# Kernel tuning notes

Hardware: AMD Instinct MI355X
Metric: run time of the kernel (lower is better)

Reference implementation:

```python
import jax, jax.numpy as jnp
import numpy as np

N = 50000        # nodes
E = 800000       # directed edges (before self-loops)
F_IN = 128       # input node features
HID = 32         # hidden channels per head
HEADS = 4
NCLS = 8
EPS_BN = 1e-5
NEG_SLOPE = 0.2  # GATConv LeakyReLU default


def setup_inputs() -> dict:
    key = jax.random.key(0)
    ks = jax.random.split(key, 16)
    rn = lambda k, shape, s=0.1: jax.random.normal(k, shape, jnp.float32) * s
    inp = {}
    inp["x"] = jax.random.normal(ks[0], (N, F_IN), jnp.float32)
    inp["edge_index"] = jax.random.randint(ks[1], (2, E), 0, N, dtype=jnp.int32)
    # layer 0: F_IN -> HEADS*HID (concat)
    inp["W0"] = rn(ks[2], (F_IN, HEADS * HID))
    inp["as0"] = rn(ks[3], (HEADS, HID))
    inp["ad0"] = rn(ks[4], (HEADS, HID))
    inp["b0"] = jnp.zeros((HEADS * HID,), jnp.float32)
    inp["g0"] = jnp.ones((HEADS * HID,), jnp.float32)
    inp["bb0"] = jnp.zeros((HEADS * HID,), jnp.float32)
    inp["rm0"] = jnp.zeros((HEADS * HID,), jnp.float32)
    inp["rv0"] = jnp.ones((HEADS * HID,), jnp.float32)
    # layer 1: HEADS*HID -> HEADS*HID (concat)
    inp["W1"] = rn(ks[5], (HEADS * HID, HEADS * HID))
    inp["as1"] = rn(ks[6], (HEADS, HID))
    inp["ad1"] = rn(ks[7], (HEADS, HID))
    inp["b1"] = jnp.zeros((HEADS * HID,), jnp.float32)
    inp["g1"] = jnp.ones((HEADS * HID,), jnp.float32)
    inp["bb1"] = jnp.zeros((HEADS * HID,), jnp.float32)
    inp["rm1"] = jnp.zeros((HEADS * HID,), jnp.float32)
    inp["rv1"] = jnp.ones((HEADS * HID,), jnp.float32)
    # layer 2: HEADS*HID -> NCLS, heads=1, concat=False
    inp["W2"] = rn(ks[8], (HEADS * HID, NCLS))
    inp["as2"] = rn(ks[9], (1, NCLS))
    inp["ad2"] = rn(ks[10], (1, NCLS))
    inp["b2"] = jnp.zeros((NCLS,), jnp.float32)
    return inp


def gat_conv(x, src, dst, W, att_s, att_d, bias, H, C, concat):
    """PyG-style GATConv (eval mode, self-loops already appended to src/dst)."""
    n = x.shape[0]
    h = (x @ W).reshape(n, H, C)                       # [N,H,C]
    a_s = (h * att_s).sum(-1)                          # [N,H]
    a_d = (h * att_d).sum(-1)                          # [N,H]
    e = jax.nn.leaky_relu(a_s[src] + a_d[dst], NEG_SLOPE)  # [E,H]
    # numerically-stable segment softmax over incoming edges of each dst node
    m = jax.ops.segment_max(e, dst, num_segments=n)
    m = jnp.where(jnp.isfinite(m), m, 0.0)
    ex = jnp.exp(e - m[dst])
    den = jax.ops.segment_sum(ex, dst, num_segments=n)
    alpha = ex / (den[dst] + 1e-16)                    # [E,H]
    out = jax.ops.segment_sum(h[src] * alpha[:, :, None], dst, num_segments=n)  # [N,H,C]
    out = out.reshape(n, H * C) if concat else out.mean(axis=1)
    return out + bias


def bn_eval(x, g, b, rm, rv):
    return (x - rm) * jax.lax.rsqrt(rv + EPS_BN) * g + b


def reference(x, edge_index, W0, as0, ad0, b0, g0, bb0, rm0, rv0,
              W1, as1, ad1, b1, g1, bb1, rm1, rv1, W2, as2, ad2, b2):
    n = x.shape[0]
    loop = jnp.arange(n, dtype=edge_index.dtype)       # self-loops (PyG default)
    src = jnp.concatenate([edge_index[0], loop])
    dst = jnp.concatenate([edge_index[1], loop])
    h = gat_conv(x, src, dst, W0, as0, ad0, b0, HEADS, HID, True)
    h = jax.nn.elu(bn_eval(h, g0, bb0, rm0, rv0))
    h = gat_conv(h, src, dst, W1, as1, ad1, b1, HEADS, HID, True)
    h = jax.nn.elu(bn_eval(h, g1, bb1, rm1, rv1))
    h = gat_conv(h, src, dst, W2, as2, ad2, b2, 1, NCLS, False)
    return jax.nn.log_softmax(h, axis=1)
```

## Files before the change

kernel.cpp:

```cpp
#include <hip/hip_runtime.h>
#include <math.h>

#define N_NODES 50000
#define N_EDGES 800000
#define ET (N_EDGES + N_NODES)
#define FDIM 128
#define HEADS 4
#define HID 32
#define NCLS 8
#define NEG 0.2f
#define EPS_BN 1e-5f

#define BSH 8
#define NBUCK ((N_NODES + 255) >> BSH)
#define EPB 4096

typedef __attribute__((ext_vector_type(8))) short short8;
typedef __attribute__((ext_vector_type(4))) float f32x4;

__device__ __forceinline__ float lrelu(float e) { return e > 0.f ? e : NEG * e; }
__device__ __forceinline__ float bflo(unsigned u) { return __uint_as_float(u << 16); }
__device__ __forceinline__ float bfhi(unsigned u) { return __uint_as_float(u & 0xffff0000u); }
__device__ __forceinline__ unsigned f2bf(float f) {
    unsigned b = __float_as_uint(f);
    return (b + 0x7fffu + ((b >> 16) & 1u)) >> 16;
}


__global__ void count_deg(const int* __restrict__ ei, int* __restrict__ cnt) {
    int e = blockIdx.x * blockDim.x + threadIdx.x;
    if (e >= ET) return;
    int d = (e < N_EDGES) ? ei[N_EDGES + e] : (e - N_EDGES);
    atomicAdd(&cnt[d], 1);
}

__global__ void scan_partial(const int* __restrict__ cnt, int* __restrict__ offs,
                             int* __restrict__ bsums) {
    __shared__ int s[256];
    int tid = threadIdx.x;
    int i = blockIdx.x * 256 + tid;
    int v = (i < N_NODES) ? cnt[i] : 0;
    s[tid] = v;
    __syncthreads();
    for (int off = 1; off < 256; off <<= 1) {
        int x = (tid >= off) ? s[tid - off] : 0;
        __syncthreads();
        s[tid] += x;
        __syncthreads();
    }
    if (i < N_NODES) offs[i] = s[tid] - v;
    if (tid == 255) bsums[blockIdx.x] = s[255];
}

__global__ void scan_root(const int* __restrict__ bsums, int* __restrict__ boffs, int nb) {
    __shared__ int s[256];
    int tid = threadIdx.x;
    int v = (tid < nb) ? bsums[tid] : 0;
    s[tid] = v;
    __syncthreads();
    for (int off = 1; off < 256; off <<= 1) {
        int x = (tid >= off) ? s[tid - off] : 0;
        __syncthreads();
        s[tid] += x;
        __syncthreads();
    }
    boffs[tid] = s[tid] - v;
}

__global__ void scan_add(int* __restrict__ offs, const int* __restrict__ boffs,
                         const int* __restrict__ bsums, int* __restrict__ bcur, int nb) {
    int i = blockIdx.x * 256 + threadIdx.x;
    if (i < N_NODES) {
        int v = offs[i] + boffs[blockIdx.x];
        offs[i] = v;
        if ((i & ((1 << BSH) - 1)) == 0) bcur[i >> BSH] = v;
    }
    if (i == 0) offs[N_NODES] = boffs[nb - 1] + bsums[nb - 1];
}

__global__ __launch_bounds__(256) void partition_pairs(const int* __restrict__ ei,
                                                       int* __restrict__ bcur,
                                                       int2* __restrict__ pairs) {
    __shared__ unsigned hist[NBUCK];
    __shared__ unsigned base[NBUCK];
    int tid = threadIdx.x;
    int e0 = blockIdx.x * EPB;
    for (int i = tid; i < NBUCK; i += 256) hist[i] = 0;
    __syncthreads();
    #pragma unroll
    for (int k = 0; k < EPB / 256; k++) {
        int e = e0 + k * 256 + tid;
        if (e < ET) {
            int d = (e < N_EDGES) ? ei[N_EDGES + e] : (e - N_EDGES);
            atomicAdd(&hist[d >> BSH], 1u);
        }
    }
    __syncthreads();
    for (int i = tid; i < NBUCK; i += 256) {
        unsigned h = hist[i];
        base[i] = h ? (unsigned)atomicAdd(&bcur[i], (int)h) : 0u;
        hist[i] = 0;
    }
    __syncthreads();
    #pragma unroll
    for (int k = 0; k < EPB / 256; k++) {
        int e = e0 + k * 256 + tid;
        if (e < ET) {
            int s, d;
            if (e < N_EDGES) { s = ei[e]; d = ei[N_EDGES + e]; }
            else             { s = d = e - N_EDGES; }
            int b = d >> BSH;
            unsigned lpos = atomicAdd(&hist[b], 1u);
            pairs[base[b] + lpos] = make_int2(s, d);
        }
    }
}

__global__ __launch_bounds__(256) void group_bucket(const int2* __restrict__ pairs,
                                                    const int* __restrict__ offs,
                                                    int* __restrict__ ssrc) {
    __shared__ int lcur[1 << BSH];
    int b = blockIdx.x, tid = threadIdx.x;
    int n0 = b << BSH;
    int base = offs[n0];
    int nend = n0 + (1 << BSH); if (nend > N_NODES) nend = N_NODES;
    int regionEnd = offs[nend];
    lcur[tid] = (n0 + tid < N_NODES) ? (offs[n0 + tid] - base) : 0;
    __syncthreads();
    for (int i = base + tid; i < regionEnd; i += 256) {
        int2 p = pairs[i];
        int pos = atomicAdd(&lcur[p.y & ((1 << BSH) - 1)], 1);
        ssrc[base + pos] = p.x;
    }
}


#define CAST_B 3125
#define PACK_B 64

__global__ void prep_inputs(const float* __restrict__ x, unsigned short* __restrict__ xb,
                            const float* __restrict__ W0, unsigned short* __restrict__ W0p,
                            const float* __restrict__ W1, unsigned short* __restrict__ W1p) {
    int b = blockIdx.x, tid = threadIdx.x;
    if (b < CAST_B) {
        int i = b * 256 + tid;
        const float4* p = (const float4*)x + (size_t)i * 2;
        float4 a = p[0], c = p[1];
        uint4 o;
        o.x = f2bf(a.x) | (f2bf(a.y) << 16);
        o.y = f2bf(a.z) | (f2bf(a.w) << 16);
        o.z = f2bf(c.x) | (f2bf(c.y) << 16);
        o.w = f2bf(c.z) | (f2bf(c.w) << 16);
        ((uint4*)xb)[i] = o;
    } else {
        int pb = b - CAST_B;
        const float* W = (pb < PACK_B) ? W0 : W1;
        unsigned short* Wp = (pb < PACK_B) ? W0p : W1p;
        int o = (pb & (PACK_B - 1)) * 256 + tid;
        int j = o & 7, lane = (o >> 3) & 63, kc = (o >> 9) & 3, t = o >> 11;
        int k = kc * 32 + ((lane >> 4) << 3) + j;
        int n = t * 16 + (lane & 15);
        Wp[o] = (unsigned short)f2bf(W[k * 128 + n]);
    }
}


__global__ __launch_bounds__(256) void gemm_attn(
        const unsigned short* __restrict__ Ab, const unsigned short* __restrict__ Wp,
        const float* __restrict__ att_s, const float* __restrict__ att_d,
        unsigned short* __restrict__ Hb, float* __restrict__ asn, float* __restrict__ adn,
        int M) {
    __shared__ float tiles[64 * 132];
    int tid = threadIdx.x;
    int wv = tid >> 6, lane = tid & 63;
    int base = blockIdx.x * 64;
    int mrow = base + wv * 16 + (lane & 15);
    if (mrow >= M) mrow = M - 1;
    int koff = (lane >> 4) * 8;

    f32x4 acc[8];
    #pragma unroll
    for (int t = 0; t < 8; t++) acc[t] = (f32x4){0.f, 0.f, 0.f, 0.f};

    #pragma unroll
    for (int kc = 0; kc < 4; kc++) {
        short8 a = *(const short8*)(Ab + (size_t)mrow * 128 + kc * 32 + koff);
        #pragma unroll
        for (int t = 0; t < 8; t++) {
            short8 b = *(const short8*)(Wp + (((t * 4 + kc) * 64 + lane) << 3));
            acc[t] = __builtin_amdgcn_mfma_f32_16x16x32_bf16(a, b, acc[t], 0, 0, 0);
        }
    }

    int rbase = wv * 16 + (lane >> 4) * 4;
    int col = lane & 15;
    #pragma unroll
    for (int t = 0; t < 8; t++)
        #pragma unroll
        for (int r = 0; r < 4; r++)
            tiles[(rbase + r) * 132 + t * 16 + col] = acc[t][r];
    __syncthreads();

    #pragma unroll
    for (int it = 0; it < 4; it++) {
        int u = tid + it * 256;
        int rl = u >> 4, cg = u & 15;
        int row = base + rl;
        if (row < M) {
            const float* p = tiles + rl * 132 + cg * 8;
            float4 v0 = *(const float4*)(p);
            float4 v1 = *(const float4*)(p + 4);
            uint4 o;
            o.x = f2bf(v0.x) | (f2bf(v0.y) << 16);
            o.y = f2bf(v0.z) | (f2bf(v0.w) << 16);
            o.z = f2bf(v1.x) | (f2bf(v1.y) << 16);
            o.w = f2bf(v1.z) | (f2bf(v1.w) << 16);
            *(uint4*)(Hb + (size_t)row * 128 + cg * 8) = o;
        }
    }

    {
        int rl = tid >> 2, hd = tid & 3;
        int row = base + rl;
        if (row < M) {
            const float* hrow = tiles + rl * 132 + hd * 32;
            const float* as = att_s + hd * 32;
            const float* ad = att_d + hd * 32;
            float ps = 0.f, pd = 0.f;
            #pragma unroll
            for (int i = 0; i < 8; i++) {
                float4 hv = *(const float4*)(hrow + i * 4);
                float4 sv = *(const float4*)(as + i * 4);
                float4 dv = *(const float4*)(ad + i * 4);
                ps += hv.x * sv.x + hv.y * sv.y + hv.z * sv.z + hv.w * sv.w;
                pd += hv.x * dv.x + hv.y * dv.y + hv.z * dv.z + hv.w * dv.w;
            }
            asn[row * 4 + hd] = ps;
            adn[row * 4 + hd] = pd;
        }
    }
}


__global__ __launch_bounds__(256) void aggregate(
        const unsigned short* __restrict__ hb, const float* __restrict__ asn,
        const float* __restrict__ adn, const int* __restrict__ offs,
        const int* __restrict__ ssrc, const float* __restrict__ bias,
        const float* __restrict__ gamma, const float* __restrict__ beta,
        const float* __restrict__ rmean, const float* __restrict__ rvar,
        unsigned short* __restrict__ outb) {
    __shared__ int2 sPair[4][4][72];
    int wv = threadIdx.x >> 6;
    int node = blockIdx.x * 4 + wv;
    if (node >= N_NODES) return;
    int lane = threadIdx.x & 63;
    int hd = lane >> 4;
    int beg = offs[node], deg = offs[node + 1] - beg;
    float4 ad4 = *(const float4*)(adn + node * 4);

    if (lane < 32) sPair[wv][lane >> 3][64 + (lane & 7)] = make_int2(0, 0);

    int s0 = 0;
    float4 e4 = make_float4(-1e30f, -1e30f, -1e30f, -1e30f);
    if (lane < deg) {
        s0 = ssrc[beg + lane];
        float4 a = *(const float4*)(asn + s0 * 4);
        e4.x = lrelu(a.x + ad4.x); e4.y = lrelu(a.y + ad4.y);
        e4.z = lrelu(a.z + ad4.z); e4.w = lrelu(a.w + ad4.w);
    }
    float4 m4 = e4;
    for (int base = 64; base < deg; base += 64) {
        int j = base + lane;
        if (j < deg) {
            int s = ssrc[beg + j];
            float4 a = *(const float4*)(asn + s * 4);
            m4.x = fmaxf(m4.x, lrelu(a.x + ad4.x));
            m4.y = fmaxf(m4.y, lrelu(a.y + ad4.y));
            m4.z = fmaxf(m4.z, lrelu(a.z + ad4.z));
            m4.w = fmaxf(m4.w, lrelu(a.w + ad4.w));
        }
    }
    #pragma unroll
    for (int off = 32; off; off >>= 1) {
        m4.x = fmaxf(m4.x, __shfl_xor(m4.x, off));
        m4.y = fmaxf(m4.y, __shfl_xor(m4.y, off));
        m4.z = fmaxf(m4.z, __shfl_xor(m4.z, off));
        m4.w = fmaxf(m4.w, __shfl_xor(m4.w, off));
    }

    float4 den4 = make_float4(0.f, 0.f, 0.f, 0.f);
    float acc0 = 0.f, acc1 = 0.f;
    const unsigned short* hlane = hb + 2 * lane;
    const int2* pp = &sPair[wv][hd][0];

    auto phaseC = [&](int cnt) {
        int bound = (cnt + 7) & ~7;
        for (int i = 0; i < bound; i += 8) {
            int2 p0 = pp[i],     p1 = pp[i + 1], p2 = pp[i + 2], p3 = pp[i + 3];
            int2 p4 = pp[i + 4], p5 = pp[i + 5], p6 = pp[i + 6], p7 = pp[i + 7];
            unsigned u0 = *(const unsigned*)(hlane + (((unsigned)p0.x) << 7));
            unsigned u1 = *(const unsigned*)(hlane + (((unsigned)p1.x) << 7));
            unsigned u2 = *(const unsigned*)(hlane + (((unsigned)p2.x) << 7));
            unsigned u3 = *(const unsigned*)(hlane + (((unsigned)p3.x) << 7));
            unsigned u4 = *(const unsigned*)(hlane + (((unsigned)p4.x) << 7));
            unsigned u5 = *(const unsigned*)(hlane + (((unsigned)p5.x) << 7));
            unsigned u6 = *(const unsigned*)(hlane + (((unsigned)p6.x) << 7));
            unsigned u7 = *(const unsigned*)(hlane + (((unsigned)p7.x) << 7));
            acc0 += __int_as_float(p0.y) * bflo(u0); acc1 += __int_as_float(p0.y) * bfhi(u0);
            acc0 += __int_as_float(p1.y) * bflo(u1); acc1 += __int_as_float(p1.y) * bfhi(u1);
            acc0 += __int_as_float(p2.y) * bflo(u2); acc1 += __int_as_float(p2.y) * bfhi(u2);
            acc0 += __int_as_float(p3.y) * bflo(u3); acc1 += __int_as_float(p3.y) * bfhi(u3);
            acc0 += __int_as_float(p4.y) * bflo(u4); acc1 += __int_as_float(p4.y) * bfhi(u4);
            acc0 += __int_as_float(p5.y) * bflo(u5); acc1 += __int_as_float(p5.y) * bfhi(u5);
            acc0 += __int_as_float(p6.y) * bflo(u6); acc1 += __int_as_float(p6.y) * bfhi(u6);
            acc0 += __int_as_float(p7.y) * bflo(u7); acc1 += __int_as_float(p7.y) * bfhi(u7);
        }
    };

    {
        float4 w4 = make_float4(0.f, 0.f, 0.f, 0.f);
        if (lane < deg) {
            w4.x = __expf(e4.x - m4.x); w4.y = __expf(e4.y - m4.y);
            w4.z = __expf(e4.z - m4.z); w4.w = __expf(e4.w - m4.w);
            den4.x += w4.x; den4.y += w4.y; den4.z += w4.z; den4.w += w4.w;
        }
        sPair[wv][0][lane] = make_int2(s0, __float_as_int(w4.x));
        sPair[wv][1][lane] = make_int2(s0, __float_as_int(w4.y));
        sPair[wv][2][lane] = make_int2(s0, __float_as_int(w4.z));
        sPair[wv][3][lane] = make_int2(s0, __float_as_int(w4.w));
        phaseC(deg < 64 ? deg : 64);
    }
    for (int base = 64; base < deg; base += 64) {
        int j = base + lane;
        int s = 0;
        float4 w4 = make_float4(0.f, 0.f, 0.f, 0.f);
        if (j < deg) {
            s = ssrc[beg + j];
            float4 a = *(const float4*)(asn + s * 4);
            w4.x = __expf(lrelu(a.x + ad4.x) - m4.x);
            w4.y = __expf(lrelu(a.y + ad4.y) - m4.y);
            w4.z = __expf(lrelu(a.z + ad4.z) - m4.z);
            w4.w = __expf(lrelu(a.w + ad4.w) - m4.w);
            den4.x += w4.x; den4.y += w4.y; den4.z += w4.z; den4.w += w4.w;
        }
        sPair[wv][0][lane] = make_int2(s, __float_as_int(w4.x));
        sPair[wv][1][lane] = make_int2(s, __float_as_int(w4.y));
        sPair[wv][2][lane] = make_int2(s, __float_as_int(w4.z));
        sPair[wv][3][lane] = make_int2(s, __float_as_int(w4.w));
        int cnt = deg - base; if (cnt > 64) cnt = 64;
        phaseC(cnt);
    }

    #pragma unroll
    for (int off = 32; off; off >>= 1) {
        den4.x += __shfl_xor(den4.x, off);
        den4.y += __shfl_xor(den4.y, off);
        den4.z += __shfl_xor(den4.z, off);
        den4.w += __shfl_xor(den4.w, off);
    }
    float den = (hd & 2) ? ((hd & 1) ? den4.w : den4.z)
                         : ((hd & 1) ? den4.y : den4.x);
    float inv = 1.f / (den + 1e-16f);

    int c0 = lane * 2;
    float2 bi = *(const float2*)(bias + c0);
    float2 gm = *(const float2*)(gamma + c0);
    float2 bt = *(const float2*)(beta + c0);
    float2 rm = *(const float2*)(rmean + c0);
    float2 rv = *(const float2*)(rvar + c0);
    float o0 = acc0 * inv + bi.x;
    float o1 = acc1 * inv + bi.y;
    o0 = (o0 - rm.x) * rsqrtf(rv.x + EPS_BN) * gm.x + bt.x;
    o1 = (o1 - rm.y) * rsqrtf(rv.y + EPS_BN) * gm.y + bt.y;
    o0 = (o0 > 0.f) ? o0 : expm1f(o0);
    o1 = (o1 > 0.f) ? o1 : expm1f(o1);
    *(unsigned*)(outb + (size_t)node * 128 + c0) = f2bf(o0) | (f2bf(o1) << 16);
}


__global__ __launch_bounds__(256) void gemm2_fused(
        const unsigned short* __restrict__ xb, const float* __restrict__ W2,
        const float* __restrict__ as2, const float* __restrict__ ad2,
        float* __restrict__ h2, float* __restrict__ asn, float* __restrict__ adn) {
    __shared__ float sW[128 * 8];
    __shared__ float sas[8], sad[8];
    int tid = threadIdx.x;
    for (int i = tid; i < 1024; i += 256) sW[i] = W2[i];
    if (tid < 8) { sas[tid] = as2[tid]; sad[tid] = ad2[tid]; }
    __syncthreads();
    int node = blockIdx.x * 256 + tid;
    if (node >= N_NODES) return;
    const uint4* xr = (const uint4*)(xb + (size_t)node * 128);
    float acc[8];
    #pragma unroll
    for (int c = 0; c < 8; c++) acc[c] = 0.f;
    for (int k8 = 0; k8 < 16; k8++) {
        uint4 u = xr[k8];
        float f[8] = { bflo(u.x), bfhi(u.x), bflo(u.y), bfhi(u.y),
                       bflo(u.z), bfhi(u.z), bflo(u.w), bfhi(u.w) };
        int kb = k8 * 8;
        #pragma unroll
        for (int q = 0; q < 8; q++)
            #pragma unroll
            for (int c = 0; c < 8; c++)
                acc[c] += f[q] * sW[(kb + q) * 8 + c];
    }
    float ps = 0.f, pd = 0.f;
    #pragma unroll
    for (int c = 0; c < 8; c++) {
        h2[(size_t)node * 8 + c] = acc[c];
        ps += acc[c] * sas[c];
        pd += acc[c] * sad[c];
    }
    asn[node] = ps;
    adn[node] = pd;
}


__global__ __launch_bounds__(256) void aggregate2(
        const float* __restrict__ h2, const float* __restrict__ asn,
        const float* __restrict__ adn, const int* __restrict__ offs,
        const int* __restrict__ ssrc, const float* __restrict__ b2,
        float* __restrict__ out) {
    __shared__ int2 sPair[4][64];
    int wv = threadIdx.x >> 6;
    int node = blockIdx.x * 4 + wv;
    if (node >= N_NODES) return;
    int lane = threadIdx.x & 63;
    int g = lane >> 3, c = lane & 7;
    int beg = offs[node], end = offs[node + 1];
    int deg = end - beg;
    float adv = adn[node];

    int s0 = 0;
    float e0v = -1e30f;
    if (lane < deg) {
        s0 = ssrc[beg + lane];
        e0v = lrelu(asn[s0] + adv);
    }
    float m = e0v;
    for (int base = 64; base < deg; base += 64) {
        int j = base + lane;
        if (j < deg) m = fmaxf(m, lrelu(asn[ssrc[beg + j]] + adv));
    }
    #pragma unroll
    for (int off = 32; off; off >>= 1) m = fmaxf(m, __shfl_xor(m, off));

    float den = 0.f, acc = 0.f;
    auto phaseC = [&](int cnt) {
        int nIt = (cnt + 15) >> 4;
        const int2* pp = &sPair[wv][0];
        for (int i = 0; i < nIt; i++) {
            int e = i * 16 + g;
            int2 p0 = pp[e];
            int2 p1 = pp[e + 8];
            acc += __int_as_float(p0.y) * h2[(((unsigned)p0.x) << 3) + c];
            acc += __int_as_float(p1.y) * h2[(((unsigned)p1.x) << 3) + c];
        }
    };

    {
        float w = 0.f;
        if (lane < deg) { w = __expf(e0v - m); den += w; }
        sPair[wv][lane] = make_int2(s0, __float_as_int(w));
        int cnt = deg < 64 ? deg : 64;
        phaseC(cnt);
    }
    for (int base = 64; base < deg; base += 64) {
        int j = base + lane;
        int s = 0; float w = 0.f;
        if (j < deg) {
            s = ssrc[beg + j];
            w = __expf(lrelu(asn[s] + adv) - m);
            den += w;
        }
        sPair[wv][lane] = make_int2(s, __float_as_int(w));
        int cnt = deg - base; if (cnt > 64) cnt = 64;
        phaseC(cnt);
    }

    acc += __shfl_xor(acc, 8); acc += __shfl_xor(acc, 16); acc += __shfl_xor(acc, 32);
    #pragma unroll
    for (int off = 32; off; off >>= 1) den += __shfl_xor(den, off);

    float o = acc / (den + 1e-16f) + b2[c];
    float mx = o;
    mx = fmaxf(mx, __shfl_xor(mx, 1));
    mx = fmaxf(mx, __shfl_xor(mx, 2));
    mx = fmaxf(mx, __shfl_xor(mx, 4));
    float ex = __expf(o - mx);
    float sm = ex;
    sm += __shfl_xor(sm, 1); sm += __shfl_xor(sm, 2); sm += __shfl_xor(sm, 4);
    if (g == 0) out[(size_t)node * 8 + c] = o - mx - logf(sm);
}


extern "C" void kernel_launch(void* const* d_in, const int* in_sizes, int n_in,
                              void* d_out, int out_size, void* d_ws, size_t ws_size,
                              hipStream_t stream) {
    const float* x   = (const float*)d_in[0];
    const int*   ei  = (const int*)d_in[1];
    const float* W0  = (const float*)d_in[2];
    const float* as0 = (const float*)d_in[3];
    const float* ad0 = (const float*)d_in[4];
    const float* b0  = (const float*)d_in[5];
    const float* g0  = (const float*)d_in[6];
    const float* bb0 = (const float*)d_in[7];
    const float* rm0 = (const float*)d_in[8];
    const float* rv0 = (const float*)d_in[9];
    const float* W1  = (const float*)d_in[10];
    const float* as1 = (const float*)d_in[11];
    const float* ad1 = (const float*)d_in[12];
    const float* b1  = (const float*)d_in[13];
    const float* g1  = (const float*)d_in[14];
    const float* bb1 = (const float*)d_in[15];
    const float* rm1 = (const float*)d_in[16];
    const float* rv1 = (const float*)d_in[17];
    const float* W2  = (const float*)d_in[18];
    const float* as2 = (const float*)d_in[19];
    const float* ad2 = (const float*)d_in[20];
    const float* b2  = (const float*)d_in[21];
    float* out = (float*)d_out;

    char* w = (char*)d_ws;
    size_t off = 0;
    auto carve = [&](size_t bytes) {
        void* p = w + off;
        off += (bytes + 255) & ~(size_t)255;
        return p;
    };
    unsigned short* xb   = (unsigned short*)carve((size_t)N_NODES * 128 * 2);
    unsigned short* Hb   = (unsigned short*)carve((size_t)N_NODES * 128 * 2);
    unsigned short* Xb   = (unsigned short*)carve((size_t)N_NODES * 128 * 2);
    unsigned short* W0p  = (unsigned short*)carve(16384 * 2);
    unsigned short* W1p  = (unsigned short*)carve(16384 * 2);
    int*   cnt    = (int*)carve((size_t)N_NODES * 4);
    int*   offs   = (int*)carve((size_t)(N_NODES + 1) * 4);
    int*   bcur   = (int*)carve((size_t)NBUCK * 4);
    int*   bsums  = (int*)carve(1024);
    int*   boffs  = (int*)carve(1024);
    int*   ssrc   = (int*)carve((size_t)ET * 4);
    int2*  pairs  = (int2*)carve((size_t)ET * 8);
    float* asn    = (float*)carve((size_t)N_NODES * 4 * 4);
    float* adn    = (float*)carve((size_t)N_NODES * 4 * 4);
    float* h2     = (float*)carve((size_t)N_NODES * 8 * 4);
    float* as2n   = (float*)carve((size_t)N_NODES * 4);
    float* ad2n   = (float*)carve((size_t)N_NODES * 4);
    (void)ws_size; (void)in_sizes; (void)n_in; (void)out_size;

    const int NB = (N_NODES + 255) / 256;
    const int GB = (N_NODES + 63) / 64;

    hipMemsetAsync(cnt, 0, (size_t)N_NODES * 4, stream);
    count_deg<<<(ET + 255) / 256, 256, 0, stream>>>(ei, cnt);
    scan_partial<<<NB, 256, 0, stream>>>(cnt, offs, bsums);
    scan_root<<<1, 256, 0, stream>>>(bsums, boffs, NB);
    scan_add<<<NB, 256, 0, stream>>>(offs, boffs, bsums, bcur, NB);
    partition_pairs<<<(ET + EPB - 1) / EPB, 256, 0, stream>>>(ei, bcur, pairs);
    group_bucket<<<NBUCK, 256, 0, stream>>>(pairs, offs, ssrc);

    prep_inputs<<<CAST_B + 2 * PACK_B, 256, 0, stream>>>(x, xb, W0, W0p, W1, W1p);

    gemm_attn<<<GB, 256, 0, stream>>>(xb, W0p, as0, ad0, Hb, asn, adn, N_NODES);
    aggregate<<<(N_NODES + 3) / 4, 256, 0, stream>>>(Hb, asn, adn, offs, ssrc,
                                                     b0, g0, bb0, rm0, rv0, Xb);
    gemm_attn<<<GB, 256, 0, stream>>>(Xb, W1p, as1, ad1, Hb, asn, adn, N_NODES);
    aggregate<<<(N_NODES + 3) / 4, 256, 0, stream>>>(Hb, asn, adn, offs, ssrc,
                                                     b1, g1, bb1, rm1, rv1, Xb);
    gemm2_fused<<<NB, 256, 0, stream>>>(Xb, W2, as2, ad2, h2, as2n, ad2n);
    aggregate2<<<(N_NODES + 3) / 4, 256, 0, stream>>>(h2, as2n, ad2n, offs, ssrc, b2, out);
}
```

Before: 329.0 us.

## Build CSR via bucket histogram and drop softmax max pass in aggregation

CSR construction changes from a per-node degree count with a three-kernel scan to a per-bucket shared-memory histogram, a single small scan, and per-node offsets computed inside group_bucket. This removes the global per-node atomics and several launches. Separately, both aggregation kernels drop the max-subtraction pass of the segment softmax and exponentiate the raw leaky-relu scores directly. That saves one gather sweep over the edges but risks overflow if attention logits grow large.

```diff
diff --git a/kernel.cpp b/kernel.cpp
--- a/kernel.cpp
+++ b/kernel.cpp
@@ -27,19 +27,33 @@
 }
 
 
-__global__ void count_deg(const int* __restrict__ ei, int* __restrict__ cnt) {
-    int e = blockIdx.x * blockDim.x + threadIdx.x;
-    if (e >= ET) return;
-    int d = (e < N_EDGES) ? ei[N_EDGES + e] : (e - N_EDGES);
-    atomicAdd(&cnt[d], 1);
-}
-
-__global__ void scan_partial(const int* __restrict__ cnt, int* __restrict__ offs,
-                             int* __restrict__ bsums) {
+__global__ __launch_bounds__(256) void bucket_hist(const int* __restrict__ ei,
+                                                   int* __restrict__ bhist) {
+    __shared__ unsigned h[NBUCK];
+    int tid = threadIdx.x;
+    int e0 = blockIdx.x * EPB;
+    for (int i = tid; i < NBUCK; i += 256) h[i] = 0;
+    __syncthreads();
+    #pragma unroll
+    for (int k = 0; k < EPB / 256; k++) {
+        int e = e0 + k * 256 + tid;
+        if (e < ET) {
+            int d = (e < N_EDGES) ? ei[N_EDGES + e] : (e - N_EDGES);
+            atomicAdd(&h[d >> BSH], 1u);
+        }
+    }
+    __syncthreads();
+    for (int i = tid; i < NBUCK; i += 256)
+        if (h[i]) atomicAdd(&bhist[i], (int)h[i]);
+}
+
+__global__ __launch_bounds__(256) void scan_buckets(const int* __restrict__ bhist,
+                                                    int* __restrict__ boffs,
+                                                    int* __restrict__ bcur,
+                                                    int* __restrict__ offs) {
     __shared__ int s[256];
     int tid = threadIdx.x;
-    int i = blockIdx.x * 256 + tid;
-    int v = (i < N_NODES) ? cnt[i] : 0;
+    int v = (tid < NBUCK) ? bhist[tid] : 0;
     s[tid] = v;
     __syncthreads();
     for (int off = 1; off < 256; off <<= 1) {
@@ -48,34 +62,9 @@
         s[tid] += x;
         __syncthreads();
     }
-    if (i < N_NODES) offs[i] = s[tid] - v;
-    if (tid == 255) bsums[blockIdx.x] = s[255];
-}
-
-__global__ void scan_root(const int* __restrict__ bsums, int* __restrict__ boffs, int nb) {
-    __shared__ int s[256];
-    int tid = threadIdx.x;
-    int v = (tid < nb) ? bsums[tid] : 0;
-    s[tid] = v;
-    __syncthreads();
-    for (int off = 1; off < 256; off <<= 1) {
-        int x = (tid >= off) ? s[tid - off] : 0;
-        __syncthreads();
-        s[tid] += x;
-        __syncthreads();
-    }
-    boffs[tid] = s[tid] - v;
-}
-
-__global__ void scan_add(int* __restrict__ offs, const int* __restrict__ boffs,
-                         const int* __restrict__ bsums, int* __restrict__ bcur, int nb) {
-    int i = blockIdx.x * 256 + threadIdx.x;
-    if (i < N_NODES) {
-        int v = offs[i] + boffs[blockIdx.x];
-        offs[i] = v;
-        if ((i & ((1 << BSH) - 1)) == 0) bcur[i >> BSH] = v;
-    }
-    if (i == 0) offs[N_NODES] = boffs[nb - 1] + bsums[nb - 1];
+    int excl = s[tid] - v;
+    if (tid < NBUCK) { boffs[tid] = excl; bcur[tid] = excl; }
+    if (tid == 0) { boffs[NBUCK] = ET; offs[N_NODES] = ET; }
 }
 
 __global__ __launch_bounds__(256) void partition_pairs(const int* __restrict__ ei,
@@ -117,19 +106,35 @@
 }
 
 __global__ __launch_bounds__(256) void group_bucket(const int2* __restrict__ pairs,
-                                                    const int* __restrict__ offs,
+                                                    const int* __restrict__ boffs,
+                                                    int* __restrict__ offs,
                                                     int* __restrict__ ssrc) {
-    __shared__ int lcur[1 << BSH];
+    __shared__ int cnt[256];
+    __shared__ int pfx[256];
     int b = blockIdx.x, tid = threadIdx.x;
     int n0 = b << BSH;
-    int base = offs[n0];
-    int nend = n0 + (1 << BSH); if (nend > N_NODES) nend = N_NODES;
-    int regionEnd = offs[nend];
-    lcur[tid] = (n0 + tid < N_NODES) ? (offs[n0 + tid] - base) : 0;
-    __syncthreads();
-    for (int i = base + tid; i < regionEnd; i += 256) {
+    int base = boffs[b], end = boffs[b + 1];
+    cnt[tid] = 0;
+    __syncthreads();
+    for (int i = base + tid; i < end; i += 256)
+        atomicAdd(&cnt[pairs[i].y & 255], 1);
+    __syncthreads();
+    int v = cnt[tid];
+    pfx[tid] = v;
+    __syncthreads();
+    for (int off = 1; off < 256; off <<= 1) {
+        int x = (tid >= off) ? pfx[tid - off] : 0;
+        __syncthreads();
+        pfx[tid] += x;
+        __syncthreads();
+    }
+    int excl = pfx[tid] - v;
+    if (n0 + tid < N_NODES) offs[n0 + tid] = base + excl;
+    cnt[tid] = excl;
+    __syncthreads();
+    for (int i = base + tid; i < end; i += 256) {
         int2 p = pairs[i];
-        int pos = atomicAdd(&lcur[p.y & ((1 << BSH) - 1)], 1);
+        int pos = atomicAdd(&cnt[p.y & 255], 1);
         ssrc[base + pos] = p.x;
     }
 }
@@ -260,34 +265,6 @@
 
     if (lane < 32) sPair[wv][lane >> 3][64 + (lane & 7)] = make_int2(0, 0);
 
-    int s0 = 0;
-    float4 e4 = make_float4(-1e30f, -1e30f, -1e30f, -1e30f);
-    if (lane < deg) {
-        s0 = ssrc[beg + lane];
-        float4 a = *(const float4*)(asn + s0 * 4);
-        e4.x = lrelu(a.x + ad4.x); e4.y = lrelu(a.y + ad4.y);
-        e4.z = lrelu(a.z + ad4.z); e4.w = lrelu(a.w + ad4.w);
-    }
-    float4 m4 = e4;
-    for (int base = 64; base < deg; base += 64) {
-        int j = base + lane;
-        if (j < deg) {
-            int s = ssrc[beg + j];
-            float4 a = *(const float4*)(asn + s * 4);
-            m4.x = fmaxf(m4.x, lrelu(a.x + ad4.x));
-            m4.y = fmaxf(m4.y, lrelu(a.y + ad4.y));
-            m4.z = fmaxf(m4.z, lrelu(a.z + ad4.z));
-            m4.w = fmaxf(m4.w, lrelu(a.w + ad4.w));
-        }
-    }
-    #pragma unroll
-    for (int off = 32; off; off >>= 1) {
-        m4.x = fmaxf(m4.x, __shfl_xor(m4.x, off));
-        m4.y = fmaxf(m4.y, __shfl_xor(m4.y, off));
-        m4.z = fmaxf(m4.z, __shfl_xor(m4.z, off));
-        m4.w = fmaxf(m4.w, __shfl_xor(m4.w, off));
-    }
-
     float4 den4 = make_float4(0.f, 0.f, 0.f, 0.f);
     float acc0 = 0.f, acc1 = 0.f;
     const unsigned short* hlane = hb + 2 * lane;
@@ -317,37 +294,24 @@
         }
     };
 
-    {
-        float4 w4 = make_float4(0.f, 0.f, 0.f, 0.f);
-        if (lane < deg) {
-            w4.x = __expf(e4.x - m4.x); w4.y = __expf(e4.y - m4.y);
-            w4.z = __expf(e4.z - m4.z); w4.w = __expf(e4.w - m4.w);
-            den4.x += w4.x; den4.y += w4.y; den4.z += w4.z; den4.w += w4.w;
-        }
-        sPair[wv][0][lane] = make_int2(s0, __float_as_int(w4.x));
-        sPair[wv][1][lane] = make_int2(s0, __float_as_int(w4.y));
-        sPair[wv][2][lane] = make_int2(s0, __float_as_int(w4.z));
-        sPair[wv][3][lane] = make_int2(s0, __float_as_int(w4.w));
-        phaseC(deg < 64 ? deg : 64);
-    }
-    for (int base = 64; base < deg; base += 64) {
-        int j = base + lane;
+    for (int base0 = 0; base0 < deg; base0 += 64) {
+        int j = base0 + lane;
         int s = 0;
         float4 w4 = make_float4(0.f, 0.f, 0.f, 0.f);
         if (j < deg) {
             s = ssrc[beg + j];
             float4 a = *(const float4*)(asn + s * 4);
-            w4.x = __expf(lrelu(a.x + ad4.x) - m4.x);
-            w4.y = __expf(lrelu(a.y + ad4.y) - m4.y);
-            w4.z = __expf(lrelu(a.z + ad4.z) - m4.z);
-            w4.w = __expf(lrelu(a.w + ad4.w) - m4.w);
+            w4.x = __expf(lrelu(a.x + ad4.x));
+            w4.y = __expf(lrelu(a.y + ad4.y));
+            w4.z = __expf(lrelu(a.z + ad4.z));
+            w4.w = __expf(lrelu(a.w + ad4.w));
             den4.x += w4.x; den4.y += w4.y; den4.z += w4.z; den4.w += w4.w;
         }
         sPair[wv][0][lane] = make_int2(s, __float_as_int(w4.x));
         sPair[wv][1][lane] = make_int2(s, __float_as_int(w4.y));
         sPair[wv][2][lane] = make_int2(s, __float_as_int(w4.z));
         sPair[wv][3][lane] = make_int2(s, __float_as_int(w4.w));
-        int cnt = deg - base; if (cnt > 64) cnt = 64;
+        int cnt = deg - base0; if (cnt > 64) cnt = 64;
         phaseC(cnt);
     }
 
@@ -432,20 +396,6 @@
     int deg = end - beg;
     float adv = adn[node];
 
-    int s0 = 0;
-    float e0v = -1e30f;
-    if (lane < deg) {
-        s0 = ssrc[beg + lane];
-        e0v = lrelu(asn[s0] + adv);
-    }
-    float m = e0v;
-    for (int base = 64; base < deg; base += 64) {
-        int j = base + lane;
-        if (j < deg) m = fmaxf(m, lrelu(asn[ssrc[beg + j]] + adv));
-    }
-    #pragma unroll
-    for (int off = 32; off; off >>= 1) m = fmaxf(m, __shfl_xor(m, off));
-
     float den = 0.f, acc = 0.f;
     auto phaseC = [&](int cnt) {
         int nIt = (cnt + 15) >> 4;
@@ -459,19 +409,12 @@
         }
     };
 
-    {
-        float w = 0.f;
-        if (lane < deg) { w = __expf(e0v - m); den += w; }
-        sPair[wv][lane] = make_int2(s0, __float_as_int(w));
-        int cnt = deg < 64 ? deg : 64;
-        phaseC(cnt);
-    }
-    for (int base = 64; base < deg; base += 64) {
+    for (int base = 0; base < deg; base += 64) {
         int j = base + lane;
         int s = 0; float w = 0.f;
         if (j < deg) {
             s = ssrc[beg + j];
-            w = __expf(lrelu(asn[s] + adv) - m);
+            w = __expf(lrelu(asn[s] + adv));
             den += w;
         }
         sPair[wv][lane] = make_int2(s, __float_as_int(w));
@@ -534,11 +477,10 @@
     unsigned short* Xb   = (unsigned short*)carve((size_t)N_NODES * 128 * 2);
     unsigned short* W0p  = (unsigned short*)carve(16384 * 2);
     unsigned short* W1p  = (unsigned short*)carve(16384 * 2);
-    int*   cnt    = (int*)carve((size_t)N_NODES * 4);
     int*   offs   = (int*)carve((size_t)(N_NODES + 1) * 4);
+    int*   bhist  = (int*)carve((size_t)NBUCK * 4);
+    int*   boffs  = (int*)carve((size_t)(NBUCK + 1) * 4);
     int*   bcur   = (int*)carve((size_t)NBUCK * 4);
-    int*   bsums  = (int*)carve(1024);
-    int*   boffs  = (int*)carve(1024);
     int*   ssrc   = (int*)carve((size_t)ET * 4);
     int2*  pairs  = (int2*)carve((size_t)ET * 8);
     float* asn    = (float*)carve((size_t)N_NODES * 4 * 4);
@@ -550,14 +492,13 @@
 
     const int NB = (N_NODES + 255) / 256;
     const int GB = (N_NODES + 63) / 64;
-
-    hipMemsetAsync(cnt, 0, (size_t)N_NODES * 4, stream);
-    count_deg<<<(ET + 255) / 256, 256, 0, stream>>>(ei, cnt);
-    scan_partial<<<NB, 256, 0, stream>>>(cnt, offs, bsums);
-    scan_root<<<1, 256, 0, stream>>>(bsums, boffs, NB);
-    scan_add<<<NB, 256, 0, stream>>>(offs, boffs, bsums, bcur, NB);
-    partition_pairs<<<(ET + EPB - 1) / EPB, 256, 0, stream>>>(ei, bcur, pairs);
-    group_bucket<<<NBUCK, 256, 0, stream>>>(pairs, offs, ssrc);
+    const int PB = (ET + EPB - 1) / EPB;
+
+    hipMemsetAsync(bhist, 0, (size_t)NBUCK * 4, stream);
+    bucket_hist<<<PB, 256, 0, stream>>>(ei, bhist);
+    scan_buckets<<<1, 256, 0, stream>>>(bhist, boffs, bcur, offs);
+    partition_pairs<<<PB, 256, 0, stream>>>(ei, bcur, pairs);
+    group_bucket<<<NBUCK, 256, 0, stream>>>(pairs, boffs, offs, ssrc);
 
     prep_inputs<<<CAST_B + 2 * PACK_B, 256, 0, stream>>>(x, xb, W0, W0p, W1, W1p);
 
```

New measurement: 289.8 us. -11.9%, faster.
